# Kernel optimization log

Hardware: AMD Instinct MI355X
Metric: run time of the kernel (lower is better)

The kernel has to match this reference:

```python
import jax, jax.numpy as jnp
import numpy as np

EPS = 1e-10

def setup_inputs() -> dict:
    key = jax.random.key(0)
    k1, k2 = jax.random.split(key)
    support_set = jax.random.normal(k1, (8192, 1024), dtype=jnp.float32)
    input_image = jax.random.normal(k2, (2048, 1024), dtype=jnp.float32)
    return {"support_set": support_set, "input_image": input_image}

def reference(support_set, input_image):
    # support_set: [n, d], input_image: [b, d]
    # Faithful to original: input magnitude is a single scalar over the whole
    # [b, d] input matrix; support magnitude is a scalar per support vector.
    input_mag = jax.lax.rsqrt(jnp.maximum(jnp.sum(input_image * input_image), EPS))  # scalar
    support_mag = jax.lax.rsqrt(jnp.maximum(jnp.sum(support_set * support_set, axis=1), EPS))  # [n]
    dot = jnp.einsum('bd,nd->nb', input_image, support_set)  # [n, b]
    sims = dot * support_mag[:, None] * input_mag  # [n, b]
    return sims[:, :, None]  # [n, b, 1] == torch.stack(...)[n,b,1].squeeze(1) (no-op for b>1)
```

## Files before the change

### kernel.cpp

```cpp
#include <hip/hip_runtime.h>
#include <hip/hip_bf16.h>
#include <stdint.h>
#include <stddef.h>

#define M_DIM 8192
#define N_DIM 2048
#define K_DIM 1024

#define BM 128
#define BN 128
#define BK 64

typedef __attribute__((ext_vector_type(8))) short short8;
typedef __attribute__((ext_vector_type(4))) float float4v;

static __device__ __forceinline__ unsigned short f2bf(float x) {
  union { float f; unsigned u; } c; c.f = x;
  return (unsigned short)((c.u + 0x7FFFu + ((c.u >> 16) & 1u)) >> 16);
}

#define GLOAD_LDS16(g, l)                                           \
  __builtin_amdgcn_global_load_lds(                                 \
      (const __attribute__((address_space(1))) void*)(g),           \
      (__attribute__((address_space(3))) void*)(l), 16, 0, 0)

__global__ __launch_bounds__(256) void prep(
    const float* __restrict__ S, const float* __restrict__ I,
    unsigned short* __restrict__ Sb, unsigned short* __restrict__ Ib,
    float* __restrict__ smag, float* __restrict__ partials) {
  const int t = threadIdx.x;
  const int blk = blockIdx.x;
  const bool isS = blk < M_DIM;
  const int row = isS ? blk : blk - M_DIM;
  const float* src = (isS ? S : I) + (size_t)row * K_DIM;
  unsigned short* dst = (isS ? Sb : Ib) + (size_t)row * K_DIM;

  const float4 v = reinterpret_cast<const float4*>(src)[t];
  ushort4 b;
  b.x = f2bf(v.x); b.y = f2bf(v.y); b.z = f2bf(v.z); b.w = f2bf(v.w);
  reinterpret_cast<ushort4*>(dst)[t] = b;

  float ss = v.x * v.x + v.y * v.y + v.z * v.z + v.w * v.w;
#pragma unroll
  for (int m = 32; m >= 1; m >>= 1) ss += __shfl_xor(ss, m, 64);
  __shared__ float wsum[4];
  if ((t & 63) == 0) wsum[t >> 6] = ss;
  __syncthreads();
  if (t == 0) {
    const float tot = wsum[0] + wsum[1] + wsum[2] + wsum[3];
    if (isS) smag[row] = rsqrtf(fmaxf(tot, 1e-10f));
    else     partials[row] = tot;
  }
}

__global__ __launch_bounds__(256) void gemm_bt(
    const unsigned short* __restrict__ A,
    const unsigned short* __restrict__ B,
    const float* __restrict__ smag,
    const float* __restrict__ partials,
    float* __restrict__ C) {
  __shared__ unsigned short lA[BM * BK];
  __shared__ unsigned short lB[BN * BK];
  __shared__ float wsum[4];

  const int t = threadIdx.x;
  const int lane = t & 63;
  const int wave = t >> 6;
  const int wr = wave >> 1;
  const int wc = wave & 1;

  const int blk = blockIdx.x;
  const int xcd = blk & 7;
  const int slot = blk >> 3;
  const int bn = (slot >> 3) * BN;
  const int bm = (xcd * 8 + (slot & 7)) * BM;

  {
    float p = 0.f;
#pragma unroll
    for (int i = 0; i < 2048 / 256; ++i) p += partials[t + i * 256];
#pragma unroll
    for (int m = 32; m >= 1; m >>= 1) p += __shfl_xor(p, m, 64);
    if ((t & 63) == 0) wsum[t >> 6] = p;
  }

  const int rsub = lane >> 3;
  const int kcg = (lane & 7) ^ (rsub & 7);
  const unsigned short* gA[4];
  const unsigned short* gB[4];
  unsigned short* dA[4];
  unsigned short* dB[4];
#pragma unroll
  for (int i = 0; i < 4; ++i) {
    const int row = i * 32 + wave * 8 + rsub;
    gA[i] = A + (size_t)(bm + row) * K_DIM + kcg * 8;
    gB[i] = B + (size_t)(bn + row) * K_DIM + kcg * 8;
    dA[i] = lA + (size_t)(i * 256 + wave * 64) * 8;
    dB[i] = lB + (size_t)(i * 256 + wave * 64) * 8;
  }

  const int fr = lane & 15;
  const int q = lane >> 4;
  const unsigned short* rA = lA + (wr * 64 + fr) * BK;
  const unsigned short* rB = lB + (wc * 64 + fr) * BK;
  const int sw = fr & 7;

  float4v acc[4][4];
#pragma unroll
  for (int i = 0; i < 4; ++i)
#pragma unroll
    for (int j = 0; j < 4; ++j) acc[i][j] = (float4v)0.0f;

  for (int kt = 0; kt < K_DIM / BK; ++kt) {
#pragma unroll
    for (int i = 0; i < 4; ++i) GLOAD_LDS16(gA[i], dA[i]);
#pragma unroll
    for (int i = 0; i < 4; ++i) GLOAD_LDS16(gB[i], dB[i]);
#pragma unroll
    for (int i = 0; i < 4; ++i) { gA[i] += BK; gB[i] += BK; }
    __syncthreads();

#pragma unroll
    for (int s = 0; s < 2; ++s) {
      const int pc = ((4 * s + q) ^ sw) * 8;
      short8 af[4], bfr[4];
#pragma unroll
      for (int i = 0; i < 4; ++i)
        af[i] = *reinterpret_cast<const short8*>(rA + i * 16 * BK + pc);
#pragma unroll
      for (int j = 0; j < 4; ++j)
        bfr[j] = *reinterpret_cast<const short8*>(rB + j * 16 * BK + pc);
#pragma unroll
      for (int i = 0; i < 4; ++i)
#pragma unroll
        for (int j = 0; j < 4; ++j)
          acc[i][j] = __builtin_amdgcn_mfma_f32_16x16x32_bf16(af[i], bfr[j], acc[i][j], 0, 0, 0);
    }
    __syncthreads();
  }

  const float imag = rsqrtf(fmaxf(wsum[0] + wsum[1] + wsum[2] + wsum[3], 1e-10f));
#pragma unroll
  for (int i = 0; i < 4; ++i) {
    const int rbase = bm + wr * 64 + i * 16 + q * 4;
#pragma unroll
    for (int r = 0; r < 4; ++r) {
      const int row = rbase + r;
      const float s = smag[row] * imag;
      float* crow = C + (size_t)row * N_DIM + bn + wc * 64 + fr;
#pragma unroll
      for (int j = 0; j < 4; ++j) crow[j * 16] = acc[i][j][r] * s;
    }
  }
}

extern "C" void kernel_launch(void* const* d_in, const int* in_sizes, int n_in,
                              void* d_out, int out_size, void* d_ws, size_t ws_size,
                              hipStream_t stream) {
  const float* S = (const float*)d_in[0];
  const float* I = (const float*)d_in[1];
  float* out = (float*)d_out;

  unsigned char* ws = (unsigned char*)d_ws;
  unsigned short* Sb = (unsigned short*)ws;
  unsigned short* Ib = (unsigned short*)(ws + (size_t)M_DIM * K_DIM * 2);
  float* smag = (float*)(ws + (size_t)M_DIM * K_DIM * 2 + (size_t)N_DIM * K_DIM * 2);
  float* partials = smag + M_DIM;

  hipLaunchKernelGGL(prep, dim3(M_DIM + N_DIM), dim3(256), 0, stream,
                     S, I, Sb, Ib, smag, partials);
  hipLaunchKernelGGL(gemm_bt, dim3((M_DIM / BM) * (N_DIM / BN)), dim3(256), 0, stream,
                     Sb, Ib, smag, partials, out);
}
```

Measured before the change: 134.7 us.

## Double-buffer LDS tiles with register prefetch and padded rows

Replaces the direct global-to-LDS loads (with XOR swizzle and two barriers per K step) by a register-staged prefetch. The next K tile is loaded into registers while MFMAs run on the current LDS buffer, then written to the alternate buffer. BK shrinks to 32 and LDS rows are padded to 40 elements to avoid bank conflicts, leaving one barrier per iteration. This aims to overlap global-memory latency with compute, at the cost of more registers and twice as many loop iterations.

```diff
diff --git a/kernel.cpp b/kernel.cpp
--- a/kernel.cpp
+++ b/kernel.cpp
@@ -9,7 +9,8 @@
 
 #define BM 128
 #define BN 128
-#define BK 64
+#define BK 32
+#define LROW 40
 
 typedef __attribute__((ext_vector_type(8))) short short8;
 typedef __attribute__((ext_vector_type(4))) float float4v;
@@ -18,11 +19,6 @@
   union { float f; unsigned u; } c; c.f = x;
   return (unsigned short)((c.u + 0x7FFFu + ((c.u >> 16) & 1u)) >> 16);
 }
-
-#define GLOAD_LDS16(g, l)                                           \
-  __builtin_amdgcn_global_load_lds(                                 \
-      (const __attribute__((address_space(1))) void*)(g),           \
-      (__attribute__((address_space(3))) void*)(l), 16, 0, 0)
 
 __global__ __launch_bounds__(256) void prep(
     const float* __restrict__ S, const float* __restrict__ I,
@@ -59,8 +55,8 @@
     const float* __restrict__ smag,
     const float* __restrict__ partials,
     float* __restrict__ C) {
-  __shared__ unsigned short lA[BM * BK];
-  __shared__ unsigned short lB[BN * BK];
+  __shared__ unsigned short lA[2][BM * LROW];
+  __shared__ unsigned short lB[2][BN * LROW];
   __shared__ float wsum[4];
 
   const int t = threadIdx.x;
@@ -84,26 +80,20 @@
     if ((t & 63) == 0) wsum[t >> 6] = p;
   }
 
-  const int rsub = lane >> 3;
-  const int kcg = (lane & 7) ^ (rsub & 7);
-  const unsigned short* gA[4];
-  const unsigned short* gB[4];
-  unsigned short* dA[4];
-  unsigned short* dB[4];
-#pragma unroll
-  for (int i = 0; i < 4; ++i) {
-    const int row = i * 32 + wave * 8 + rsub;
-    gA[i] = A + (size_t)(bm + row) * K_DIM + kcg * 8;
-    gB[i] = B + (size_t)(bn + row) * K_DIM + kcg * 8;
-    dA[i] = lA + (size_t)(i * 256 + wave * 64) * 8;
-    dB[i] = lB + (size_t)(i * 256 + wave * 64) * 8;
-  }
+  const int pr0 = t >> 2;
+  const int pc = (t & 3);
+  const int pr1 = pr0 + 64;
+  const unsigned short* gA0 = A + (size_t)(bm + pr0) * K_DIM + pc * 8;
+  const unsigned short* gA1 = A + (size_t)(bm + pr1) * K_DIM + pc * 8;
+  const unsigned short* gB0 = B + (size_t)(bn + pr0) * K_DIM + pc * 8;
+  const unsigned short* gB1 = B + (size_t)(bn + pr1) * K_DIM + pc * 8;
+  const int w0 = pr0 * LROW + pc * 8;
+  const int w1 = pr1 * LROW + pc * 8;
 
   const int fr = lane & 15;
   const int q = lane >> 4;
-  const unsigned short* rA = lA + (wr * 64 + fr) * BK;
-  const unsigned short* rB = lB + (wc * 64 + fr) * BK;
-  const int sw = fr & 7;
+  const int rAo = (wr * 64 + fr) * LROW + q * 8;
+  const int rBo = (wc * 64 + fr) * LROW + q * 8;
 
   float4v acc[4][4];
 #pragma unroll
@@ -111,32 +101,47 @@
 #pragma unroll
     for (int j = 0; j < 4; ++j) acc[i][j] = (float4v)0.0f;
 
+  uint4 ra0 = *reinterpret_cast<const uint4*>(gA0);
+  uint4 ra1 = *reinterpret_cast<const uint4*>(gA1);
+  uint4 rb0 = *reinterpret_cast<const uint4*>(gB0);
+  uint4 rb1 = *reinterpret_cast<const uint4*>(gB1);
+  gA0 += BK; gA1 += BK; gB0 += BK; gB1 += BK;
+  *reinterpret_cast<uint4*>(&lA[0][w0]) = ra0;
+  *reinterpret_cast<uint4*>(&lA[0][w1]) = ra1;
+  *reinterpret_cast<uint4*>(&lB[0][w0]) = rb0;
+  *reinterpret_cast<uint4*>(&lB[0][w1]) = rb1;
+
+#pragma unroll 2
   for (int kt = 0; kt < K_DIM / BK; ++kt) {
+    __syncthreads();
+    const int p = kt & 1;
+    if (kt < K_DIM / BK - 1) {
+      ra0 = *reinterpret_cast<const uint4*>(gA0);
+      ra1 = *reinterpret_cast<const uint4*>(gA1);
+      rb0 = *reinterpret_cast<const uint4*>(gB0);
+      rb1 = *reinterpret_cast<const uint4*>(gB1);
+      gA0 += BK; gA1 += BK; gB0 += BK; gB1 += BK;
+    }
+
+    short8 af[4], bf[4];
 #pragma unroll
-    for (int i = 0; i < 4; ++i) GLOAD_LDS16(gA[i], dA[i]);
+    for (int i = 0; i < 4; ++i)
+      af[i] = *reinterpret_cast<const short8*>(&lA[p][rAo + i * 16 * LROW]);
 #pragma unroll
-    for (int i = 0; i < 4; ++i) GLOAD_LDS16(gB[i], dB[i]);
+    for (int j = 0; j < 4; ++j)
+      bf[j] = *reinterpret_cast<const short8*>(&lB[p][rBo + j * 16 * LROW]);
 #pragma unroll
-    for (int i = 0; i < 4; ++i) { gA[i] += BK; gB[i] += BK; }
-    __syncthreads();
-
-#pragma unroll
-    for (int s = 0; s < 2; ++s) {
-      const int pc = ((4 * s + q) ^ sw) * 8;
-      short8 af[4], bfr[4];
-#pragma unroll
-      for (int i = 0; i < 4; ++i)
-        af[i] = *reinterpret_cast<const short8*>(rA + i * 16 * BK + pc);
+    for (int i = 0; i < 4; ++i)
 #pragma unroll
       for (int j = 0; j < 4; ++j)
-        bfr[j] = *reinterpret_cast<const short8*>(rB + j * 16 * BK + pc);
-#pragma unroll
-      for (int i = 0; i < 4; ++i)
-#pragma unroll
-        for (int j = 0; j < 4; ++j)
-          acc[i][j] = __builtin_amdgcn_mfma_f32_16x16x32_bf16(af[i], bfr[j], acc[i][j], 0, 0, 0);
+        acc[i][j] = __builtin_amdgcn_mfma_f32_16x16x32_bf16(af[i], bf[j], acc[i][j], 0, 0, 0);
+
+    if (kt < K_DIM / BK - 1) {
+      *reinterpret_cast<uint4*>(&lA[p ^ 1][w0]) = ra0;
+      *reinterpret_cast<uint4*>(&lA[p ^ 1][w1]) = ra1;
+      *reinterpret_cast<uint4*>(&lB[p ^ 1][w0]) = rb0;
+      *reinterpret_cast<uint4*>(&lB[p ^ 1][w1]) = rb1;
     }
-    __syncthreads();
   }
 
   const float imag = rsqrtf(fmaxf(wsum[0] + wsum[1] + wsum[2] + wsum[3], 1e-10f));
```

Result: slower. 143.5 us (+6.6%).

## Prefetch next K tile into registers to overlap global loads with MFMA

Applied to the files above, without the earlier changes.

Replaces direct global-to-LDS loads with register-staged loads. The next K tile is issued into registers before the MFMAs on the current tile and written to LDS after the barrier. This overlaps global memory latency with compute in a single-buffered LDS scheme, at the cost of extra VGPRs and explicit LDS store instructions.

```diff
diff --git a/kernel.cpp b/kernel.cpp
--- a/kernel.cpp
+++ b/kernel.cpp
@@ -18,11 +18,6 @@
   union { float f; unsigned u; } c; c.f = x;
   return (unsigned short)((c.u + 0x7FFFu + ((c.u >> 16) & 1u)) >> 16);
 }
-
-#define GLOAD_LDS16(g, l)                                           \
-  __builtin_amdgcn_global_load_lds(                                 \
-      (const __attribute__((address_space(1))) void*)(g),           \
-      (__attribute__((address_space(3))) void*)(l), 16, 0, 0)
 
 __global__ __launch_bounds__(256) void prep(
     const float* __restrict__ S, const float* __restrict__ I,
@@ -84,20 +79,17 @@
     if ((t & 63) == 0) wsum[t >> 6] = p;
   }
 
-  const int rsub = lane >> 3;
-  const int kcg = (lane & 7) ^ (rsub & 7);
+  const int kcg = (t & 7) ^ ((t >> 3) & 7);
+  const int r0 = t >> 3;
   const unsigned short* gA[4];
   const unsigned short* gB[4];
-  unsigned short* dA[4];
-  unsigned short* dB[4];
-#pragma unroll
-  for (int i = 0; i < 4; ++i) {
-    const int row = i * 32 + wave * 8 + rsub;
-    gA[i] = A + (size_t)(bm + row) * K_DIM + kcg * 8;
-    gB[i] = B + (size_t)(bn + row) * K_DIM + kcg * 8;
-    dA[i] = lA + (size_t)(i * 256 + wave * 64) * 8;
-    dB[i] = lB + (size_t)(i * 256 + wave * 64) * 8;
-  }
+#pragma unroll
+  for (int i = 0; i < 4; ++i) {
+    gA[i] = A + (size_t)(bm + r0 + 32 * i) * K_DIM + kcg * 8;
+    gB[i] = B + (size_t)(bn + r0 + 32 * i) * K_DIM + kcg * 8;
+  }
+  unsigned short* wAp = lA + (size_t)t * 8;
+  unsigned short* wBp = lB + (size_t)t * 8;
 
   const int fr = lane & 15;
   const int q = lane >> 4;
@@ -111,32 +103,67 @@
 #pragma unroll
     for (int j = 0; j < 4; ++j) acc[i][j] = (float4v)0.0f;
 
+  uint4 sa[4], sb[4];
+#pragma unroll
+  for (int i = 0; i < 4; ++i) {
+    sa[i] = *reinterpret_cast<const uint4*>(gA[i]);
+    sb[i] = *reinterpret_cast<const uint4*>(gB[i]);
+    gA[i] += BK; gB[i] += BK;
+  }
+#pragma unroll
+  for (int i = 0; i < 4; ++i) {
+    *reinterpret_cast<uint4*>(wAp + i * 2048) = sa[i];
+    *reinterpret_cast<uint4*>(wBp + i * 2048) = sb[i];
+  }
+
   for (int kt = 0; kt < K_DIM / BK; ++kt) {
-#pragma unroll
-    for (int i = 0; i < 4; ++i) GLOAD_LDS16(gA[i], dA[i]);
-#pragma unroll
-    for (int i = 0; i < 4; ++i) GLOAD_LDS16(gB[i], dB[i]);
-#pragma unroll
-    for (int i = 0; i < 4; ++i) { gA[i] += BK; gB[i] += BK; }
     __syncthreads();
 
-#pragma unroll
-    for (int s = 0; s < 2; ++s) {
-      const int pc = ((4 * s + q) ^ sw) * 8;
-      short8 af[4], bfr[4];
-#pragma unroll
-      for (int i = 0; i < 4; ++i)
-        af[i] = *reinterpret_cast<const short8*>(rA + i * 16 * BK + pc);
+    short8 af0[4], bf0[4];
+#pragma unroll
+    for (int i = 0; i < 4; ++i)
+      af0[i] = *reinterpret_cast<const short8*>(rA + i * 16 * BK + (q ^ sw) * 8);
+#pragma unroll
+    for (int j = 0; j < 4; ++j)
+      bf0[j] = *reinterpret_cast<const short8*>(rB + j * 16 * BK + (q ^ sw) * 8);
+
+    if (kt < K_DIM / BK - 1) {
+#pragma unroll
+      for (int i = 0; i < 4; ++i) {
+        sa[i] = *reinterpret_cast<const uint4*>(gA[i]);
+        sb[i] = *reinterpret_cast<const uint4*>(gB[i]);
+        gA[i] += BK; gB[i] += BK;
+      }
+    }
+
+#pragma unroll
+    for (int i = 0; i < 4; ++i)
 #pragma unroll
       for (int j = 0; j < 4; ++j)
-        bfr[j] = *reinterpret_cast<const short8*>(rB + j * 16 * BK + pc);
-#pragma unroll
-      for (int i = 0; i < 4; ++i)
-#pragma unroll
-        for (int j = 0; j < 4; ++j)
-          acc[i][j] = __builtin_amdgcn_mfma_f32_16x16x32_bf16(af[i], bfr[j], acc[i][j], 0, 0, 0);
+        acc[i][j] = __builtin_amdgcn_mfma_f32_16x16x32_bf16(af0[i], bf0[j], acc[i][j], 0, 0, 0);
+
+    short8 af1[4], bf1[4];
+#pragma unroll
+    for (int i = 0; i < 4; ++i)
+      af1[i] = *reinterpret_cast<const short8*>(rA + i * 16 * BK + ((4 + q) ^ sw) * 8);
+#pragma unroll
+    for (int j = 0; j < 4; ++j)
+      bf1[j] = *reinterpret_cast<const short8*>(rB + j * 16 * BK + ((4 + q) ^ sw) * 8);
+#pragma unroll
+    for (int i = 0; i < 4; ++i)
+#pragma unroll
+      for (int j = 0; j < 4; ++j)
+        acc[i][j] = __builtin_amdgcn_mfma_f32_16x16x32_bf16(af1[i], bf1[j], acc[i][j], 0, 0, 0);
+
+    __syncthreads();
+
+    if (kt < K_DIM / BK - 1) {
+#pragma unroll
+      for (int i = 0; i < 4; ++i) {
+        *reinterpret_cast<uint4*>(wAp + i * 2048) = sa[i];
+        *reinterpret_cast<uint4*>(wBp + i * 2048) = sb[i];
+      }
     }
-    __syncthreads();
   }
 
   const float imag = rsqrtf(fmaxf(wsum[0] + wsum[1] + wsum[2] + wsum[3], 1e-10f));
```

Measured after the change: 242.6 us. +80.2%, slower.
